# Kernel optimization log

Measured on AMD Instinct MI355X. Metric: run time of the kernel, lower is better.

## Reference

```python
import jax, jax.numpy as jnp
import numpy as np

ALPHA = 1.0
BETA = 10.0
MARGIN = 0.5


def setup_inputs() -> dict:
    key = jax.random.key(0)
    k1, k2 = jax.random.split(key)
    emb = jax.random.normal(k1, (4096, 512), dtype=jnp.float32)
    # module docstring: embeddings are L2-normalized
    emb = emb / jnp.linalg.norm(emb, axis=1, keepdims=True)
    labels = jax.random.randint(k2, (4096,), 0, 64, dtype=jnp.int64)
    return {"embeddings": emb, "labels": labels}


def reference(embeddings, labels):
    n = embeddings.shape[0]
    sim = embeddings @ embeddings.T  # [n, n]
    labels_eq = labels[None, :] == labels[:, None]
    eye = jnp.eye(n, dtype=bool)
    pos_mask = labels_eq & ~eye
    neg_mask = ~labels_eq & ~eye

    # masked exp-sums (masked entries contribute 0, matching torch's
    # clone/NEG_INF/zero-out dance without materializing extra copies)
    pos_exp = jnp.where(pos_mask, jnp.exp(-ALPHA * (sim - MARGIN)), 0.0)
    neg_exp = jnp.where(neg_mask, jnp.exp(BETA * (sim - MARGIN)), 0.0)
    pos_term = (1.0 / ALPHA) * jnp.log1p(pos_exp.sum(axis=1))
    neg_term = (1.0 / BETA) * jnp.log1p(neg_exp.sum(axis=1))

    valid = pos_mask.any(axis=1) & neg_mask.any(axis=1)
    n_valid = valid.sum()
    total = jnp.where(valid, pos_term + neg_term, 0.0).sum()
    return jnp.where(n_valid > 0, total / jnp.maximum(n_valid, 1).astype(sim.dtype), 0.0)
```

## Files before the change

### kernel.cpp

```cpp
#include <hip/hip_runtime.h>
#include <hip/hip_bf16.h>

#define N 4096
#define D 512
#define MARGIN 0.5f
#define BETA 10.0f

typedef __attribute__((ext_vector_type(8))) short short8;
typedef __attribute__((ext_vector_type(4))) float floatx4;

__device__ inline unsigned short f2bf(float f) {
    unsigned u = __float_as_uint(f);
    u += 0x7fffu + ((u >> 16) & 1u);
    return (unsigned short)(u >> 16);
}

__global__ __launch_bounds__(256) void convert_bf16_kernel(
        const float4* __restrict__ in, ushort4* __restrict__ out,
        float* __restrict__ sums ) {
    int idx = blockIdx.x * 256 + threadIdx.x;
    if (idx < 2 * N) sums[idx] = 0.f;
    float4 v = in[idx];
    ushort4 o;
    o.x = f2bf(v.x); o.y = f2bf(v.y); o.z = f2bf(v.z); o.w = f2bf(v.w);
    out[idx] = o;
}

__global__ __launch_bounds__(256, 4) void ms_loss_gemm(
        const unsigned short* __restrict__ Ebf,
        const int* __restrict__ labels,
        float* __restrict__ pos_sum,
        float* __restrict__ neg_sum) {
    __shared__ unsigned short Atile[128 * 32];
    __shared__ unsigned short Btile[128 * 32];
    __shared__ int rlab[128];
    __shared__ int clab[128];

    int t = blockIdx.x;
    int bi = 0;
    while (t >= (32 - bi)) { t -= (32 - bi); ++bi; }
    const int bj = bi + t;
    const bool diag = (bi == bj);

    const int tid  = threadIdx.x;
    const int wave = tid >> 6;
    const int lane = tid & 63;
    const int quad = lane >> 4;
    const int lcol = lane & 15;
    const int wrow = wave >> 1;
    const int wcol = wave & 1;
    const int ibase = bi * 128;
    const int jbase = bj * 128;

    if (tid < 128)       rlab[tid]       = labels[ibase + tid];
    else                 clab[tid - 128] = labels[jbase + tid - 128];

    floatx4 acc[4][4];
#pragma unroll
    for (int mt = 0; mt < 4; ++mt)
#pragma unroll
        for (int nt = 0; nt < 4; ++nt)
            acc[mt][nt] = (floatx4){0.f, 0.f, 0.f, 0.f};

    const char* Eb = (const char*)Ebf;
    char* Ab = (char*)Atile;
    char* Bb = (char*)Btile;
    const char* Bread = diag ? Ab : Bb;
    const int srow = lane >> 2;
    const int sckb = ((lane & 3) ^ ((lane >> 3) & 3)) * 16;
    const int rdsw = ((lcol >> 1) & 3);

    for (int kt = 0; kt < D / 32; ++kt) {
        __syncthreads();
        const int kb = kt * 64;
#pragma unroll
        for (int it = 0; it < 2; ++it) {
            int r    = wave * 16 + it * 64 + srow;
            int ldso = wave * 1024 + it * 4096 + lane * 16;
            const char* ga = Eb + (size_t)(ibase + r) * (D * 2) + kb + sckb;
            __builtin_amdgcn_global_load_lds(
                (const __attribute__((address_space(1))) void*)ga,
                (__attribute__((address_space(3))) void*)(Ab + ldso), 16, 0, 0);
            if (!diag) {
                const char* gb = Eb + (size_t)(jbase + r) * (D * 2) + kb + sckb;
                __builtin_amdgcn_global_load_lds(
                    (const __attribute__((address_space(1))) void*)gb,
                    (__attribute__((address_space(3))) void*)(Bb + ldso), 16, 0, 0);
            }
        }
        __syncthreads();

        short8 a[4], b[4];
        const int rchunk = (quad ^ rdsw) * 16;
#pragma unroll
        for (int mt = 0; mt < 4; ++mt) {
            int r = wrow * 64 + mt * 16 + lcol;
            a[mt] = *(const short8*)(Ab + r * 64 + rchunk);
        }
#pragma unroll
        for (int nt = 0; nt < 4; ++nt) {
            int c = wcol * 64 + nt * 16 + lcol;
            b[nt] = *(const short8*)(Bread + c * 64 + rchunk);
        }
#pragma unroll
        for (int mt = 0; mt < 4; ++mt)
#pragma unroll
            for (int nt = 0; nt < 4; ++nt)
                acc[mt][nt] = __builtin_amdgcn_mfma_f32_16x16x32_bf16(
                    a[mt], b[nt], acc[mt][nt], 0, 0, 0);
    }

    int ljv[4], gjv[4];
#pragma unroll
    for (int nt = 0; nt < 4; ++nt) {
        int cl = wcol * 64 + nt * 16 + lcol;
        ljv[nt] = clab[cl];
        gjv[nt] = jbase + cl;
    }

    float colp[4] = {0.f, 0.f, 0.f, 0.f};
    float coln[4] = {0.f, 0.f, 0.f, 0.f};

#pragma unroll
    for (int mt = 0; mt < 4; ++mt) {
#pragma unroll
        for (int reg = 0; reg < 4; ++reg) {
            int rl = wrow * 64 + mt * 16 + quad * 4 + reg;
            int gi = ibase + rl;
            int li = rlab[rl];
            float p = 0.f, ng = 0.f;
#pragma unroll
            for (int nt = 0; nt < 4; ++nt) {
                float s = acc[mt][nt][reg];
                if (gi != gjv[nt]) {
                    if (li == ljv[nt]) {
                        float e = __expf(MARGIN - s);
                        p += e;  colp[nt] += e;
                    } else {
                        float e = __expf(BETA * (s - MARGIN));
                        ng += e; coln[nt] += e;
                    }
                }
            }
            p  += __shfl_xor(p, 1);   ng += __shfl_xor(ng, 1);
            p  += __shfl_xor(p, 2);   ng += __shfl_xor(ng, 2);
            p  += __shfl_xor(p, 4);   ng += __shfl_xor(ng, 4);
            p  += __shfl_xor(p, 8);   ng += __shfl_xor(ng, 8);
            if (lcol == 0) {
                atomicAdd(&pos_sum[gi], p);
                atomicAdd(&neg_sum[gi], ng);
            }
        }
    }

    if (!diag) {
#pragma unroll
        for (int nt = 0; nt < 4; ++nt) {
            float cp = colp[nt], cn = coln[nt];
            cp += __shfl_xor(cp, 16);  cn += __shfl_xor(cn, 16);
            cp += __shfl_xor(cp, 32);  cn += __shfl_xor(cn, 32);
            if (quad == 0) {
                int gj = gjv[nt];
                atomicAdd(&pos_sum[gj], cp);
                atomicAdd(&neg_sum[gj], cn);
            }
        }
    }
}

__global__ __launch_bounds__(256) void finalize_kernel(
        const float4* __restrict__ pos4, const float4* __restrict__ neg4,
        float* __restrict__ out) {
    __shared__ float sb[256];
    __shared__ int   sc[256];
    const int tid = threadIdx.x;
    float tot = 0.f;
    int cnt = 0;
#pragma unroll
    for (int it = 0; it < N / 4 / 256; ++it) {
        int i = it * 256 + tid;
        float4 p = pos4[i];
        float4 ng = neg4[i];
        const float* pp = (const float*)&p;
        const float* nn = (const float*)&ng;
#pragma unroll
        for (int j = 0; j < 4; ++j) {
            if (pp[j] > 0.f && nn[j] > 0.f) {
                tot += log1pf(pp[j]) + (1.0f / BETA) * log1pf(nn[j]);
                cnt += 1;
            }
        }
    }
    sb[tid] = tot; sc[tid] = cnt;
    __syncthreads();
    for (int s = 128; s > 0; s >>= 1) {
        if (tid < s) { sb[tid] += sb[tid + s]; sc[tid] += sc[tid + s]; }
        __syncthreads();
    }
    if (tid == 0) out[0] = (sc[0] > 0) ? sb[0] / (float)sc[0] : 0.f;
}

extern "C" void kernel_launch(void* const* d_in, const int* in_sizes, int n_in,
                              void* d_out, int out_size, void* d_ws, size_t ws_size,
                              hipStream_t stream) {
    const float* emb   = (const float*)d_in[0];
    const int* labels  = (const int*)d_in[1];
    float* out         = (float*)d_out;

    char* ws = (char*)d_ws;
    unsigned short* Ebf = (unsigned short*)ws;
    float* pos_sum = (float*)(ws + (size_t)N * D * 2);
    float* neg_sum = pos_sum + N;

    convert_bf16_kernel<<<(N * D / 4) / 256, 256, 0, stream>>>(
        (const float4*)emb, (ushort4*)Ebf, pos_sum);

    ms_loss_gemm<<<(32 * 33) / 2, 256, 0, stream>>>(Ebf, labels, pos_sum, neg_sum);

    finalize_kernel<<<1, 256, 0, stream>>>(
        (const float4*)pos_sum, (const float4*)neg_sum, out);
}
```

Before: 93.16 us.

## Load MFMA operands directly from global memory into registers with double buffering

Drops the LDS staging tiles and the two barriers per k-step. Each wave now loads its A and B bf16 fragments straight from global memory into registers, prefetching the next k-slice while the MFMAs for the current slice run. Occupancy hint drops from 4 to 3 to make room for the extra registers. The cost is that operands are no longer shared through LDS, so waves read redundant data from global/L2 (each row is read by two waves) with smaller uncoalesced 16-byte row-strided accesses, and the diagonal-tile reuse of A as B is lost.

```diff
diff --git a/kernel.cpp b/kernel.cpp
--- a/kernel.cpp
+++ b/kernel.cpp
@@ -26,13 +26,11 @@
     out[idx] = o;
 }
 
-__global__ __launch_bounds__(256, 4) void ms_loss_gemm(
+__global__ __launch_bounds__(256, 3) void ms_loss_gemm(
         const unsigned short* __restrict__ Ebf,
         const int* __restrict__ labels,
         float* __restrict__ pos_sum,
         float* __restrict__ neg_sum) {
-    __shared__ unsigned short Atile[128 * 32];
-    __shared__ unsigned short Btile[128 * 32];
     __shared__ int rlab[128];
     __shared__ int clab[128];
 
@@ -54,6 +52,18 @@
 
     if (tid < 128)       rlab[tid]       = labels[ibase + tid];
     else                 clab[tid - 128] = labels[jbase + tid - 128];
+    __syncthreads();
+
+    const char* Eb = (const char*)Ebf;
+    const char* aBase[4];
+    const char* bBase[4];
+#pragma unroll
+    for (int x = 0; x < 4; ++x) {
+        int r = ibase + wrow * 64 + x * 16 + lcol;
+        int c = jbase + wcol * 64 + x * 16 + lcol;
+        aBase[x] = Eb + (size_t)r * (D * 2) + quad * 16;
+        bBase[x] = Eb + (size_t)c * (D * 2) + quad * 16;
+    }
 
     floatx4 acc[4][4];
 #pragma unroll
@@ -62,52 +72,30 @@
         for (int nt = 0; nt < 4; ++nt)
             acc[mt][nt] = (floatx4){0.f, 0.f, 0.f, 0.f};
 
-    const char* Eb = (const char*)Ebf;
-    char* Ab = (char*)Atile;
-    char* Bb = (char*)Btile;
-    const char* Bread = diag ? Ab : Bb;
-    const int srow = lane >> 2;
-    const int sckb = ((lane & 3) ^ ((lane >> 3) & 3)) * 16;
-    const int rdsw = ((lcol >> 1) & 3);
-
+    short8 abuf[2][4], bbuf[2][4];
+#pragma unroll
+    for (int x = 0; x < 4; ++x) {
+        abuf[0][x] = *(const short8*)(aBase[x]);
+        bbuf[0][x] = *(const short8*)(bBase[x]);
+    }
+
+#pragma unroll
     for (int kt = 0; kt < D / 32; ++kt) {
-        __syncthreads();
-        const int kb = kt * 64;
-#pragma unroll
-        for (int it = 0; it < 2; ++it) {
-            int r    = wave * 16 + it * 64 + srow;
-            int ldso = wave * 1024 + it * 4096 + lane * 16;
-            const char* ga = Eb + (size_t)(ibase + r) * (D * 2) + kb + sckb;
-            __builtin_amdgcn_global_load_lds(
-                (const __attribute__((address_space(1))) void*)ga,
-                (__attribute__((address_space(3))) void*)(Ab + ldso), 16, 0, 0);
-            if (!diag) {
-                const char* gb = Eb + (size_t)(jbase + r) * (D * 2) + kb + sckb;
-                __builtin_amdgcn_global_load_lds(
-                    (const __attribute__((address_space(1))) void*)gb,
-                    (__attribute__((address_space(3))) void*)(Bb + ldso), 16, 0, 0);
-            }
-        }
-        __syncthreads();
-
-        short8 a[4], b[4];
-        const int rchunk = (quad ^ rdsw) * 16;
-#pragma unroll
-        for (int mt = 0; mt < 4; ++mt) {
-            int r = wrow * 64 + mt * 16 + lcol;
-            a[mt] = *(const short8*)(Ab + r * 64 + rchunk);
-        }
-#pragma unroll
-        for (int nt = 0; nt < 4; ++nt) {
-            int c = wcol * 64 + nt * 16 + lcol;
-            b[nt] = *(const short8*)(Bread + c * 64 + rchunk);
+        const int cur = kt & 1, nxt = cur ^ 1;
+        if (kt < D / 32 - 1) {
+            const int off = (kt + 1) * 64;
+#pragma unroll
+            for (int x = 0; x < 4; ++x) {
+                abuf[nxt][x] = *(const short8*)(aBase[x] + off);
+                bbuf[nxt][x] = *(const short8*)(bBase[x] + off);
+            }
         }
 #pragma unroll
         for (int mt = 0; mt < 4; ++mt)
 #pragma unroll
             for (int nt = 0; nt < 4; ++nt)
                 acc[mt][nt] = __builtin_amdgcn_mfma_f32_16x16x32_bf16(
-                    a[mt], b[nt], acc[mt][nt], 0, 0, 0);
+                    abuf[cur][mt], bbuf[cur][nt], acc[mt][nt], 0, 0, 0);
     }
 
     int ljv[4], gjv[4];
```

After: 120.2 us. +29.0%, slower.

## Prefetch next K-tile into registers instead of direct global-to-LDS loads

Applied to the files above, without the earlier changes.

Replaces the direct global_load_lds copies with register prefetching. The next K slice is loaded into registers while the current one is written to LDS and consumed by the MFMAs, so global latency can overlap with compute in the single-buffered loop. The launch-bounds occupancy hint drops from 4 to 2 blocks per CU to leave room for the extra prefetch registers, at the cost of fewer resident waves to hide latency.

```diff
diff --git a/kernel.cpp b/kernel.cpp
--- a/kernel.cpp
+++ b/kernel.cpp
@@ -26,13 +26,13 @@
     out[idx] = o;
 }
 
-__global__ __launch_bounds__(256, 4) void ms_loss_gemm(
+__global__ __launch_bounds__(256, 2) void ms_loss_gemm(
         const unsigned short* __restrict__ Ebf,
         const int* __restrict__ labels,
         float* __restrict__ pos_sum,
         float* __restrict__ neg_sum) {
-    __shared__ unsigned short Atile[128 * 32];
-    __shared__ unsigned short Btile[128 * 32];
+    __shared__ char Als[128 * 64];
+    __shared__ char Bls[128 * 64];
     __shared__ int rlab[128];
     __shared__ int clab[128];
 
@@ -63,29 +63,37 @@
             acc[mt][nt] = (floatx4){0.f, 0.f, 0.f, 0.f};
 
     const char* Eb = (const char*)Ebf;
-    char* Ab = (char*)Atile;
-    char* Bb = (char*)Btile;
-    const char* Bread = diag ? Ab : Bb;
-    const int srow = lane >> 2;
-    const int sckb = ((lane & 3) ^ ((lane >> 3) & 3)) * 16;
-    const int rdsw = ((lcol >> 1) & 3);
+    const int srow  = wave * 16 + (lane >> 2);
+    const int schunk = lane & 3;
+    const int swz   = (lane >> 3) & 3;
+    const int ldw   = srow * 64 + (schunk ^ swz) * 16;
+    const size_t ga0 = (size_t)(ibase + srow) * 1024 + schunk * 16;
+    const size_t gb0 = (size_t)(jbase + srow) * 1024 + schunk * 16;
+
+    const int rdsw = (lcol >> 1) & 3;
+    const char* Bread = diag ? Als : Bls;
+
+    short8 pa[2], pb[2];
+#pragma unroll
+    for (int it = 0; it < 2; ++it) {
+        pa[it] = *(const short8*)(Eb + ga0 + (size_t)it * 65536);
+        if (!diag) pb[it] = *(const short8*)(Eb + gb0 + (size_t)it * 65536);
+    }
 
     for (int kt = 0; kt < D / 32; ++kt) {
         __syncthreads();
-        const int kb = kt * 64;
 #pragma unroll
         for (int it = 0; it < 2; ++it) {
-            int r    = wave * 16 + it * 64 + srow;
-            int ldso = wave * 1024 + it * 4096 + lane * 16;
-            const char* ga = Eb + (size_t)(ibase + r) * (D * 2) + kb + sckb;
-            __builtin_amdgcn_global_load_lds(
-                (const __attribute__((address_space(1))) void*)ga,
-                (__attribute__((address_space(3))) void*)(Ab + ldso), 16, 0, 0);
-            if (!diag) {
-                const char* gb = Eb + (size_t)(jbase + r) * (D * 2) + kb + sckb;
-                __builtin_amdgcn_global_load_lds(
-                    (const __attribute__((address_space(1))) void*)gb,
-                    (__attribute__((address_space(3))) void*)(Bb + ldso), 16, 0, 0);
+            *(short8*)(Als + ldw + it * 4096) = pa[it];
+            if (!diag) *(short8*)(Bls + ldw + it * 4096) = pb[it];
+        }
+        if (kt < D / 32 - 1) {
+            const size_t kb = (size_t)(kt + 1) * 64;
+#pragma unroll
+            for (int it = 0; it < 2; ++it) {
+                pa[it] = *(const short8*)(Eb + ga0 + (size_t)it * 65536 + kb);
+                if (!diag)
+                    pb[it] = *(const short8*)(Eb + gb0 + (size_t)it * 65536 + kb);
             }
         }
         __syncthreads();
@@ -95,7 +103,7 @@
 #pragma unroll
         for (int mt = 0; mt < 4; ++mt) {
             int r = wrow * 64 + mt * 16 + lcol;
-            a[mt] = *(const short8*)(Ab + r * 64 + rchunk);
+            a[mt] = *(const short8*)(Als + r * 64 + rchunk);
         }
 #pragma unroll
         for (int nt = 0; nt < 4; ++nt) {
```

Measured after the change: 95.27 us. 1.02x slower.
